# Performance work log

Hardware: AMD Instinct MI355X
Metric: run time of the kernel (lower is better)

## Reference

```python
import jax, jax.numpy as jnp
import numpy as np

ALPHA = 0.5
N_CACHE = 8
N_HEAD = 16
NUM_MODULES = 4


def _ncn_module(x, xa, W, alpha, n_cache, n_head):
    """One fused NCN module: per-head mix, alpha blend with cache slot (t % n_cache),
    activation, and cache update. x: [B,T,D], xa: [B,n_cache,D], W: [H,dh,dh]."""
    B, T, D = x.shape
    dh = D // n_head
    xh = x.reshape(B, T, n_head, dh).transpose(1, 0, 2, 3)  # [T,B,H,dh]
    cache0 = xa.reshape(B, n_cache, n_head, dh)             # [B,C,H,dh]
    slots = jnp.arange(T) % n_cache                          # cache slot per step

    def step(cache, inp):
        xt, s = inp                                          # xt: [B,H,dh]
        mix = jnp.einsum('bhd,hde->bhe', xt, W)              # per-head mixing
        y = jnp.tanh(alpha * cache[:, s] + (1.0 - alpha) * mix)
        return cache.at[:, s].set(y), y

    cache_f, ys = jax.lax.scan(step, cache0, (xh, slots))
    yi = ys.transpose(1, 0, 2, 3).reshape(B, T, D)
    ya = cache_f.reshape(B, n_cache, D)
    return yi, ya


def setup_inputs() -> dict:
    key = jax.random.key(0)
    k1, k2, k3 = jax.random.split(key, 3)
    B, T, D = 8, 4096, 1024
    dh = D // N_HEAD
    x = jax.random.normal(k1, (B, T, D), dtype=jnp.float32)
    xa = jax.random.normal(k2, (B, N_CACHE, D), dtype=jnp.float32)
    # scale weights for stable tanh recurrence
    weights = jax.random.normal(k3, (NUM_MODULES, N_HEAD, dh, dh), dtype=jnp.float32) / np.sqrt(dh)
    return {"x": x, "xa": xa, "weights": weights}


def reference(x, xa, weights):
    for m in range(NUM_MODULES):
        x, xa = _ncn_module(x, xa, weights[m], ALPHA, N_CACHE, N_HEAD)
    return x, xa
```

## Files before the change

kernel.cpp:

```cpp
#include <hip/hip_runtime.h>
#include <hip/hip_fp16.h>


typedef _Float16 f16;
typedef _Float16 half8 __attribute__((ext_vector_type(8)));
typedef _Float16 half4v __attribute__((ext_vector_type(4)));
typedef float f32x4 __attribute__((ext_vector_type(4)));
typedef unsigned uint4v __attribute__((ext_vector_type(4)));

constexpr int B = 8, T = 4096, D = 1024, H = 16, DH = 64, NC = 8, NM = 4;
constexpr int KS = 32;
constexpr int NCH = (T / NC) / KS;
constexpr size_t YWS_BYTES = (size_t)B * T * 2048;
constexpr float L2E = 1.44269504088896340736f;

__device__ __forceinline__ float exp2_fast(float v) {
  float r;
  asm("v_exp_f32 %0, %1" : "=v"(r) : "v"(v));
  return r;
}

template <bool WS>
__global__ __launch_bounds__(256, 1)
void ncn_wave(const float* __restrict__ x, const float* __restrict__ xa,
              const float* __restrict__ w, float* __restrict__ out,
              unsigned char* __restrict__ ybuf) {
  constexpr int YROW = WS ? 2048 : 4096;
  __shared__ __align__(16) unsigned char YST[4][4096];
  __shared__ __align__(16) unsigned char MXS[4][8192];

  const int tid = threadIdx.x, lane = tid & 63, wv = tid >> 6;
  const int g = blockIdx.x * 4 + wv;
  const int c = g & 7, h = (g >> 3) & 15, b = g >> 7;
  const int lr = lane & 15, lg = lane >> 4;

  unsigned char* const yst = YST[wv];
  unsigned char* const mxs = MXS[wv];
  const unsigned char* const xb = (const unsigned char*)x + (size_t)b * T * 4096;
  unsigned char* const ob = (unsigned char*)out + (size_t)b * T * 4096;
  unsigned char* const yb = ybuf + (size_t)b * T * YROW;

  float y = xa[((size_t)b * NC + c) * D + h * DH + lane];
  float u = y * L2E;

  uint4v pf[8];
  half8 Wf[4][2];

  auto prefetch = [&](int m, int ch) {
    const int J0 = ch * KS;
    if (m == 0) {
#pragma unroll
      for (int i = 0; i < 8; ++i) {
        const int lt = i * 4 + (lane >> 4);
        const int t = (J0 + lt) * 8 + c;
        pf[i] = *(const uint4v*)(xb + (size_t)t * 4096 + h * 256 + (lane & 15) * 16);
      }
    } else {
#pragma unroll
      for (int i = 0; i < 4; ++i) {
        const int lt = i * 8 + (lane >> 3);
        const int t = (J0 + lt) * 8 + c;
        pf[i] = *(const uint4v*)(yb + (size_t)t * YROW + h * 128 + (lane & 7) * 16);
      }
    }
  };
  auto stage = [&](int m) {
    if (m == 0) {
#pragma unroll
      for (int i = 0; i < 8; ++i) {
        const int lt = i * 4 + (lane >> 4);
        const f32x4 v = __builtin_bit_cast(f32x4, pf[i]);
        const __half2 p0 = __floats2half2_rn(v.x, v.y);
        const __half2 p1 = __floats2half2_rn(v.z, v.w);
        uint2 pk;
        pk.x = __builtin_bit_cast(unsigned, p0);
        pk.y = __builtin_bit_cast(unsigned, p1);
        *(uint2*)(yst + lt * 128 + (((lane & 15) * 8) ^ ((lt & 7) << 4))) = pk;
      }
    } else {
#pragma unroll
      for (int i = 0; i < 4; ++i) {
        const int lt = i * 8 + (lane >> 3);
        *(uint4v*)(yst + lt * 128 + (((lane & 7) * 16) ^ ((lt & 7) << 4))) = pf[i];
      }
    }
  };

  for (int m = 0; m < NM; ++m) {
    const float* wh = w + ((size_t)m * H + h) * DH * DH;
#pragma unroll
    for (int it = 0; it < 4; ++it)
#pragma unroll
      for (int kt = 0; kt < 2; ++kt)
#pragma unroll
        for (int j = 0; j < 8; ++j)
          Wf[it][kt][j] =
              (f16)wh[(size_t)(kt * 32 + lg * 8 + j) * DH + it * 16 + lr];

    asm volatile("s_waitcnt vmcnt(0)" ::: "memory");

    prefetch(m, 0);
    stage(m);
    prefetch(m, 1);

    for (int ch = 0; ch < NCH; ++ch) {
      f32x4 acc[2][4];
#pragma unroll
      for (int tq = 0; tq < 2; ++tq) {
        half8 Xf[2];
#pragma unroll
        for (int kt = 0; kt < 2; ++kt) {
          const int lt = tq * 16 + lr;
          Xf[kt] = *(const half8*)(yst + lt * 128 +
                                   ((kt * 64 + lg * 16) ^ ((lt & 7) << 4)));
        }
#pragma unroll
        for (int it = 0; it < 4; ++it) acc[tq][it] = (f32x4){0.f, 0.f, 0.f, 0.f};
#pragma unroll
        for (int kt = 0; kt < 2; ++kt)
#pragma unroll
          for (int it = 0; it < 4; ++it)
            acc[tq][it] = __builtin_amdgcn_mfma_f32_16x16x32_f16(
                Xf[kt], Wf[it][kt], acc[tq][it], 0, 0, 0);
      }
      asm volatile("s_waitcnt lgkmcnt(0)" ::: "memory");
      if (ch + 1 < NCH) stage(m);
      if (ch + 2 < NCH) prefetch(m, ch + 2);

#pragma unroll
      for (int tq = 0; tq < 2; ++tq)
#pragma unroll
        for (int it = 0; it < 4; ++it) {
          const int e = it * 16 + lr;
          const __half2 p0 = __floats2half2_rn(acc[tq][it].x, acc[tq][it].y);
          const __half2 p1 = __floats2half2_rn(acc[tq][it].z, acc[tq][it].w);
          uint2 pk;
          pk.x = __builtin_bit_cast(unsigned, p0);
          pk.y = __builtin_bit_cast(unsigned, p1);
          *(uint2*)(mxs + e * 128 + ((tq * 32 + lg * 8) ^ ((e & 7) << 4))) = pk;
        }
      asm volatile("s_waitcnt lgkmcnt(0)" ::: "memory");

      half8 mxr[4];
#pragma unroll
      for (int k16 = 0; k16 < 4; ++k16)
        mxr[k16] = *(const half8*)(mxs + lane * 128 +
                                   ((k16 * 16) ^ ((lane & 7) << 4)));
      float mix2[KS];
#pragma unroll
      for (int k = 0; k < KS; ++k) mix2[k] = (float)mxr[k >> 3][k & 7] * L2E;

      const int t0 = ch * KS * 8 + c;
      if (m < 3 || !WS) {
        unsigned char* sp = yb + (size_t)t0 * YROW + h * 128 + 2 * lane;
#pragma unroll
        for (int k = 0; k < KS; ++k) {
          const float z = u + mix2[k];
          const float E = exp2_fast(z);
          const float r = __builtin_amdgcn_rcpf(E + 1.0f);
          y = fmaf(r, -2.0f, 1.0f);
          u = fmaf(r, -2.0f * L2E, L2E);
          *(__half*)sp = __float2half_rn(y);
          sp += (size_t)8 * YROW;
        }
      } else {
        unsigned char* sp = ob + (size_t)t0 * 4096 + h * 256 + 4 * lane;
#pragma unroll
        for (int k = 0; k < KS; ++k) {
          const float z = u + mix2[k];
          const float E = exp2_fast(z);
          const float r = __builtin_amdgcn_rcpf(E + 1.0f);
          y = fmaf(r, -2.0f, 1.0f);
          u = fmaf(r, -2.0f * L2E, L2E);
          *(float*)sp = y;
          sp += (size_t)8 * 4096;
        }
      }
    }
  }

  float* ya = out + (size_t)B * T * D;
  ya[((size_t)b * NC + c) * D + h * DH + lane] = y;
}

__global__ __launch_bounds__(256)
void expand(float* __restrict__ buf) {
  __shared__ __align__(16) f16 rs[4 * 1024];
  const int tid = threadIdx.x;
  unsigned char* const base = (unsigned char*)buf + (size_t)blockIdx.x * 4 * 4096;
#pragma unroll
  for (int p = 0; p < 2; ++p) {
    const int gid = p * 256 + tid;
    const int row = gid >> 7, c16 = gid & 127;
    *(uint4v*)((unsigned char*)rs + row * 2048 + c16 * 16) =
        *(const uint4v*)(base + (size_t)row * 4096 + c16 * 16);
  }
  __syncthreads();
#pragma unroll
  for (int p = 0; p < 4; ++p) {
    const int gid = p * 256 + tid;
    const int row = gid >> 8, c4 = gid & 255;
    const half4v hv = *(const half4v*)((unsigned char*)rs + row * 2048 + c4 * 8);
    f32x4 v;
#pragma unroll
    for (int e = 0; e < 4; ++e) v[e] = (float)hv[e];
    *(f32x4*)(base + (size_t)row * 4096 + c4 * 16) = v;
  }
}

extern "C" void kernel_launch(void* const* d_in, const int* in_sizes, int n_in,
                              void* d_out, int out_size, void* d_ws, size_t ws_size,
                              hipStream_t stream) {
  (void)in_sizes; (void)n_in; (void)out_size;
  const float* x  = (const float*)d_in[0];
  const float* xa = (const float*)d_in[1];
  const float* w  = (const float*)d_in[2];
  float* out = (float*)d_out;

  const bool usews = (d_ws != nullptr) && (ws_size >= YWS_BYTES);
  if (usews) {
    hipLaunchKernelGGL((ncn_wave<true>), dim3(256), dim3(256), 0, stream,
                       x, xa, w, out, (unsigned char*)d_ws);
  } else {
    hipLaunchKernelGGL((ncn_wave<false>), dim3(256), dim3(256), 0, stream,
                       x, xa, w, out, (unsigned char*)out);
    hipLaunchKernelGGL(expand, dim3(B * T / 4), dim3(256), 0, stream, out);
  }
}
```

Before: 136.2 us.

## Software-pipeline MFMA mixing of next chunk with tanh scan of current

Restructures the per-chunk loop so the MFMA products for chunk ch+1 are issued before the serial tanh recurrence of chunk ch runs, with a scheduling barrier to keep them ahead. The mix results are moved to LDS and reloaded after the scan, so matrix-core latency can hide behind the latency-bound scalar recurrence. In exchange, accumulator and mix registers stay live across the scan, which raises register pressure, and the staging buffer is now written before the previous GEMM's reads are explicitly waited on.

Result: no change. 136.9 us (+0.5%).

```diff
diff --git a/kernel.cpp b/kernel.cpp
--- a/kernel.cpp
+++ b/kernel.cpp
@@ -45,6 +45,8 @@
 
   uint4v pf[8];
   half8 Wf[4][2];
+  float mixf[KS];
+  f32x4 acc[2][4];
 
   auto prefetch = [&](int m, int ch) {
     const int J0 = ch * KS;
@@ -85,6 +87,77 @@
       }
     }
   };
+  auto gemm_issue = [&]() {
+#pragma unroll
+    for (int tq = 0; tq < 2; ++tq) {
+      half8 Xf[2];
+#pragma unroll
+      for (int kt = 0; kt < 2; ++kt) {
+        const int lt = tq * 16 + lr;
+        Xf[kt] = *(const half8*)(yst + lt * 128 +
+                                 ((kt * 64 + lg * 16) ^ ((lt & 7) << 4)));
+      }
+#pragma unroll
+      for (int it = 0; it < 4; ++it) acc[tq][it] = (f32x4){0.f, 0.f, 0.f, 0.f};
+#pragma unroll
+      for (int kt = 0; kt < 2; ++kt)
+#pragma unroll
+        for (int it = 0; it < 4; ++it)
+          acc[tq][it] = __builtin_amdgcn_mfma_f32_16x16x32_f16(
+              Xf[kt], Wf[it][kt], acc[tq][it], 0, 0, 0);
+    }
+  };
+  auto scatter = [&]() {
+#pragma unroll
+    for (int tq = 0; tq < 2; ++tq)
+#pragma unroll
+      for (int it = 0; it < 4; ++it) {
+        const int e = it * 16 + lr;
+        const __half2 p0 = __floats2half2_rn(acc[tq][it].x, acc[tq][it].y);
+        const __half2 p1 = __floats2half2_rn(acc[tq][it].z, acc[tq][it].w);
+        uint2 pk;
+        pk.x = __builtin_bit_cast(unsigned, p0);
+        pk.y = __builtin_bit_cast(unsigned, p1);
+        *(uint2*)(mxs + e * 128 + ((tq * 32 + lg * 8) ^ ((e & 7) << 4))) = pk;
+      }
+  };
+  auto mixload = [&]() {
+    half8 mxr[4];
+#pragma unroll
+    for (int k16 = 0; k16 < 4; ++k16)
+      mxr[k16] = *(const half8*)(mxs + lane * 128 +
+                                 ((k16 * 16) ^ ((lane & 7) << 4)));
+#pragma unroll
+    for (int k = 0; k < KS; ++k) mixf[k] = (float)mxr[k >> 3][k & 7] * L2E;
+  };
+  auto scan = [&](int m, int ch) {
+    const int t0 = ch * KS * 8 + c;
+    if (m < 3 || !WS) {
+      unsigned char* sp = yb + (size_t)t0 * YROW + h * 128 + 2 * lane;
+#pragma unroll
+      for (int k = 0; k < KS; ++k) {
+        const float z = u + mixf[k];
+        const float E = exp2_fast(z);
+        const float r = __builtin_amdgcn_rcpf(E + 1.0f);
+        y = fmaf(r, -2.0f, 1.0f);
+        u = fmaf(r, -2.0f * L2E, L2E);
+        *(__half*)sp = __float2half_rn(y);
+        sp += (size_t)8 * YROW;
+      }
+    } else {
+      unsigned char* sp = ob + (size_t)t0 * 4096 + h * 256 + 4 * lane;
+#pragma unroll
+      for (int k = 0; k < KS; ++k) {
+        const float z = u + mixf[k];
+        const float E = exp2_fast(z);
+        const float r = __builtin_amdgcn_rcpf(E + 1.0f);
+        y = fmaf(r, -2.0f, 1.0f);
+        u = fmaf(r, -2.0f * L2E, L2E);
+        *(float*)sp = y;
+        sp += (size_t)8 * 4096;
+      }
+    }
+  };
 
   for (int m = 0; m < NM; ++m) {
     const float* wh = w + ((size_t)m * H + h) * DH * DH;
@@ -102,79 +175,24 @@
     prefetch(m, 0);
     stage(m);
     prefetch(m, 1);
+    gemm_issue();
+    scatter();
+    asm volatile("s_waitcnt lgkmcnt(0)" ::: "memory");
+    mixload();
 
     for (int ch = 0; ch < NCH; ++ch) {
-      f32x4 acc[2][4];
-#pragma unroll
-      for (int tq = 0; tq < 2; ++tq) {
-        half8 Xf[2];
-#pragma unroll
-        for (int kt = 0; kt < 2; ++kt) {
-          const int lt = tq * 16 + lr;
-          Xf[kt] = *(const half8*)(yst + lt * 128 +
-                                   ((kt * 64 + lg * 16) ^ ((lt & 7) << 4)));
-        }
-#pragma unroll
-        for (int it = 0; it < 4; ++it) acc[tq][it] = (f32x4){0.f, 0.f, 0.f, 0.f};
-#pragma unroll
-        for (int kt = 0; kt < 2; ++kt)
-#pragma unroll
-          for (int it = 0; it < 4; ++it)
-            acc[tq][it] = __builtin_amdgcn_mfma_f32_16x16x32_f16(
-                Xf[kt], Wf[it][kt], acc[tq][it], 0, 0, 0);
-      }
-      asm volatile("s_waitcnt lgkmcnt(0)" ::: "memory");
-      if (ch + 1 < NCH) stage(m);
-      if (ch + 2 < NCH) prefetch(m, ch + 2);
-
-#pragma unroll
-      for (int tq = 0; tq < 2; ++tq)
-#pragma unroll
-        for (int it = 0; it < 4; ++it) {
-          const int e = it * 16 + lr;
-          const __half2 p0 = __floats2half2_rn(acc[tq][it].x, acc[tq][it].y);
-          const __half2 p1 = __floats2half2_rn(acc[tq][it].z, acc[tq][it].w);
-          uint2 pk;
-          pk.x = __builtin_bit_cast(unsigned, p0);
-          pk.y = __builtin_bit_cast(unsigned, p1);
-          *(uint2*)(mxs + e * 128 + ((tq * 32 + lg * 8) ^ ((e & 7) << 4))) = pk;
-        }
-      asm volatile("s_waitcnt lgkmcnt(0)" ::: "memory");
-
-      half8 mxr[4];
-#pragma unroll
-      for (int k16 = 0; k16 < 4; ++k16)
-        mxr[k16] = *(const half8*)(mxs + lane * 128 +
-                                   ((k16 * 16) ^ ((lane & 7) << 4)));
-      float mix2[KS];
-#pragma unroll
-      for (int k = 0; k < KS; ++k) mix2[k] = (float)mxr[k >> 3][k & 7] * L2E;
-
-      const int t0 = ch * KS * 8 + c;
-      if (m < 3 || !WS) {
-        unsigned char* sp = yb + (size_t)t0 * YROW + h * 128 + 2 * lane;
-#pragma unroll
-        for (int k = 0; k < KS; ++k) {
-          const float z = u + mix2[k];
-          const float E = exp2_fast(z);
-          const float r = __builtin_amdgcn_rcpf(E + 1.0f);
-          y = fmaf(r, -2.0f, 1.0f);
-          u = fmaf(r, -2.0f * L2E, L2E);
-          *(__half*)sp = __float2half_rn(y);
-          sp += (size_t)8 * YROW;
-        }
-      } else {
-        unsigned char* sp = ob + (size_t)t0 * 4096 + h * 256 + 4 * lane;
-#pragma unroll
-        for (int k = 0; k < KS; ++k) {
-          const float z = u + mix2[k];
-          const float E = exp2_fast(z);
-          const float r = __builtin_amdgcn_rcpf(E + 1.0f);
-          y = fmaf(r, -2.0f, 1.0f);
-          u = fmaf(r, -2.0f * L2E, L2E);
-          *(float*)sp = y;
-          sp += (size_t)8 * 4096;
-        }
+      const bool more = (ch + 1 < NCH);
+      if (more) {
+        stage(m);
+        if (ch + 2 < NCH) prefetch(m, ch + 2);
+        gemm_issue();
+        __builtin_amdgcn_sched_barrier(0);
+      }
+      scan(m, ch);
+      if (more) {
+        scatter();
+        asm volatile("s_waitcnt lgkmcnt(0)" ::: "memory");
+        mixload();
       }
     }
   }
```

## Split each chain into producer GEMM wave and consumer recurrence wave with LDS flags

Applied to the files above, without the earlier changes.

Each (batch, head, cache-slot) chain now gets a pair of waves. One wave loads and stages inputs and runs the MFMA mixing into a double-buffered LDS mix buffer. The other wave runs the serial tanh recurrence and writes outputs, and the two hand off through workgroup-scope atomic flags. The aim is to overlap the matrix multiply and global loads with the latency-bound recurrence, which the old single wave ran back to back. In exchange the kernel launches twice as many blocks, pays for spin-wait synchronisation, and adds a dependency that blocks the next module's prefetch until the recurrence has stored its outputs.

Measured after the change: 135.4 us. About the same (-0.6%).

```diff
diff --git a/kernel.cpp b/kernel.cpp
--- a/kernel.cpp
+++ b/kernel.cpp
@@ -4,13 +4,13 @@
 
 typedef _Float16 f16;
 typedef _Float16 half8 __attribute__((ext_vector_type(8)));
-typedef _Float16 half4v __attribute__((ext_vector_type(4)));
 typedef float f32x4 __attribute__((ext_vector_type(4)));
 typedef unsigned uint4v __attribute__((ext_vector_type(4)));
 
 constexpr int B = 8, T = 4096, D = 1024, H = 16, DH = 64, NC = 8, NM = 4;
 constexpr int KS = 32;
-constexpr int NCH = (T / NC) / KS;
+constexpr int NCH = 16;
+constexpr int NG = NM * NCH;
 constexpr size_t YWS_BYTES = (size_t)B * T * 2048;
 constexpr float L2E = 1.44269504088896340736f;
 
@@ -21,89 +21,111 @@
 }
 
 template <bool WS>
-__global__ __launch_bounds__(256, 1)
-void ncn_wave(const float* __restrict__ x, const float* __restrict__ xa,
+__global__ __launch_bounds__(256, 2)
+void ncn_pair(const float* __restrict__ x, const float* __restrict__ xa,
               const float* __restrict__ w, float* __restrict__ out,
               unsigned char* __restrict__ ybuf) {
   constexpr int YROW = WS ? 2048 : 4096;
-  __shared__ __align__(16) unsigned char YST[4][4096];
-  __shared__ __align__(16) unsigned char MXS[4][8192];
+  __shared__ __align__(16) unsigned char YST[2][4096];
+  __shared__ __align__(16) unsigned char MXS[2][2][8192];
+  __shared__ int FLG[2][4];
 
   const int tid = threadIdx.x, lane = tid & 63, wv = tid >> 6;
-  const int g = blockIdx.x * 4 + wv;
+  const int pair = wv >> 1;
+  const bool gemmw = (wv & 1) == 0;
+  const int g = blockIdx.x * 2 + pair;
   const int c = g & 7, h = (g >> 3) & 15, b = g >> 7;
   const int lr = lane & 15, lg = lane >> 4;
 
-  unsigned char* const yst = YST[wv];
-  unsigned char* const mxs = MXS[wv];
   const unsigned char* const xb = (const unsigned char*)x + (size_t)b * T * 4096;
   unsigned char* const ob = (unsigned char*)out + (size_t)b * T * 4096;
   unsigned char* const yb = ybuf + (size_t)b * T * YROW;
 
-  float y = xa[((size_t)b * NC + c) * D + h * DH + lane];
-  float u = y * L2E;
-
-  uint4v pf[8];
-  half8 Wf[4][2];
-
-  auto prefetch = [&](int m, int ch) {
-    const int J0 = ch * KS;
-    if (m == 0) {
-#pragma unroll
-      for (int i = 0; i < 8; ++i) {
-        const int lt = i * 4 + (lane >> 4);
-        const int t = (J0 + lt) * 8 + c;
-        pf[i] = *(const uint4v*)(xb + (size_t)t * 4096 + h * 256 + (lane & 15) * 16);
-      }
-    } else {
-#pragma unroll
-      for (int i = 0; i < 4; ++i) {
-        const int lt = i * 8 + (lane >> 3);
-        const int t = (J0 + lt) * 8 + c;
-        pf[i] = *(const uint4v*)(yb + (size_t)t * YROW + h * 128 + (lane & 7) * 16);
-      }
-    }
+  if (tid < 8) ((int*)FLG)[tid] = 0;
+  __syncthreads();
+
+  int* const fgp = &FLG[pair][0];
+  int* const fmx = &FLG[pair][1];
+  int* const fy  = &FLG[pair][2];
+
+  auto waitge = [&](int* f, int v) {
+    while (__hip_atomic_load(f, __ATOMIC_ACQUIRE,
+                             __HIP_MEMORY_SCOPE_WORKGROUP) < v)
+      __builtin_amdgcn_s_sleep(1);
   };
-  auto stage = [&](int m) {
-    if (m == 0) {
-#pragma unroll
-      for (int i = 0; i < 8; ++i) {
-        const int lt = i * 4 + (lane >> 4);
-        const f32x4 v = __builtin_bit_cast(f32x4, pf[i]);
-        const __half2 p0 = __floats2half2_rn(v.x, v.y);
-        const __half2 p1 = __floats2half2_rn(v.z, v.w);
-        uint2 pk;
-        pk.x = __builtin_bit_cast(unsigned, p0);
-        pk.y = __builtin_bit_cast(unsigned, p1);
-        *(uint2*)(yst + lt * 128 + (((lane & 15) * 8) ^ ((lt & 7) << 4))) = pk;
-      }
-    } else {
-#pragma unroll
-      for (int i = 0; i < 4; ++i) {
-        const int lt = i * 8 + (lane >> 3);
-        *(uint4v*)(yst + lt * 128 + (((lane & 7) * 16) ^ ((lt & 7) << 4))) = pf[i];
-      }
-    }
+  auto signal = [&](int* f, int v) {
+    if (lane == 0)
+      __hip_atomic_store(f, v, __ATOMIC_RELEASE, __HIP_MEMORY_SCOPE_WORKGROUP);
   };
 
-  for (int m = 0; m < NM; ++m) {
-    const float* wh = w + ((size_t)m * H + h) * DH * DH;
-#pragma unroll
-    for (int it = 0; it < 4; ++it)
-#pragma unroll
-      for (int kt = 0; kt < 2; ++kt)
-#pragma unroll
-        for (int j = 0; j < 8; ++j)
-          Wf[it][kt][j] =
-              (f16)wh[(size_t)(kt * 32 + lg * 8 + j) * DH + it * 16 + lr];
-
-    asm volatile("s_waitcnt vmcnt(0)" ::: "memory");
-
-    prefetch(m, 0);
-    stage(m);
-    prefetch(m, 1);
-
-    for (int ch = 0; ch < NCH; ++ch) {
+  if (gemmw) {
+    unsigned char* const yst = YST[pair];
+    uint4v pf[8];
+    half8 Wf[4][2];
+
+    auto prefetch = [&](int Gn) {
+      if (Gn >= NG) return;
+      const int m = Gn >> 4, ch = Gn & 15;
+      if (m >= 1) waitge(fy, (m - 1) * 16 + ch + 1);
+      const int J0 = ch * KS;
+      if (m == 0) {
+#pragma unroll
+        for (int i = 0; i < 8; ++i) {
+          const int lt = i * 4 + (lane >> 4);
+          const int t = (J0 + lt) * 8 + c;
+          pf[i] = *(const uint4v*)(xb + (size_t)t * 4096 + h * 256 +
+                                   (lane & 15) * 16);
+        }
+      } else {
+#pragma unroll
+        for (int i = 0; i < 4; ++i) {
+          const int lt = i * 8 + (lane >> 3);
+          const int t = (J0 + lt) * 8 + c;
+          pf[i] = *(const uint4v*)(yb + (size_t)t * YROW + h * 128 +
+                                   (lane & 7) * 16);
+        }
+      }
+    };
+    auto stage = [&](int m) {
+      if (m == 0) {
+#pragma unroll
+        for (int i = 0; i < 8; ++i) {
+          const int lt = i * 4 + (lane >> 4);
+          const f32x4 v = __builtin_bit_cast(f32x4, pf[i]);
+          const __half2 p0 = __floats2half2_rn(v.x, v.y);
+          const __half2 p1 = __floats2half2_rn(v.z, v.w);
+          uint2 pk;
+          pk.x = __builtin_bit_cast(unsigned, p0);
+          pk.y = __builtin_bit_cast(unsigned, p1);
+          *(uint2*)(yst + lt * 128 + (((lane & 15) * 8) ^ ((lt & 7) << 4))) = pk;
+        }
+      } else {
+#pragma unroll
+        for (int i = 0; i < 4; ++i) {
+          const int lt = i * 8 + (lane >> 3);
+          *(uint4v*)(yst + lt * 128 + (((lane & 7) * 16) ^ ((lt & 7) << 4))) =
+              pf[i];
+        }
+      }
+    };
+
+    prefetch(0);
+    for (int G = 0; G < NG; ++G) {
+      const int m = G >> 4, ch = G & 15;
+      if (ch == 0) {
+        const float* wh = w + ((size_t)m * H + h) * DH * DH;
+#pragma unroll
+        for (int it = 0; it < 4; ++it)
+#pragma unroll
+          for (int kt = 0; kt < 2; ++kt)
+#pragma unroll
+            for (int j = 0; j < 8; ++j)
+              Wf[it][kt][j] =
+                  (f16)wh[(size_t)(kt * 32 + lg * 8 + j) * DH + it * 16 + lr];
+      }
+      stage(m);
+      prefetch(G + 1);
+
       f32x4 acc[2][4];
 #pragma unroll
       for (int tq = 0; tq < 2; ++tq) {
@@ -123,10 +145,9 @@
             acc[tq][it] = __builtin_amdgcn_mfma_f32_16x16x32_f16(
                 Xf[kt], Wf[it][kt], acc[tq][it], 0, 0, 0);
       }
-      asm volatile("s_waitcnt lgkmcnt(0)" ::: "memory");
-      if (ch + 1 < NCH) stage(m);
-      if (ch + 2 < NCH) prefetch(m, ch + 2);
-
+
+      waitge(fmx, G - 1);
+      unsigned char* const mxs = MXS[pair][G & 1];
 #pragma unroll
       for (int tq = 0; tq < 2; ++tq)
 #pragma unroll
@@ -140,22 +161,33 @@
           *(uint2*)(mxs + e * 128 + ((tq * 32 + lg * 8) ^ ((e & 7) << 4))) = pk;
         }
       asm volatile("s_waitcnt lgkmcnt(0)" ::: "memory");
-
+      signal(fgp, G + 1);
+    }
+  } else {
+    float y = xa[((size_t)b * NC + c) * D + h * DH + lane];
+    float u = y * L2E;
+    float mixf[KS];
+
+    for (int G = 0; G < NG; ++G) {
+      const int m = G >> 4, ch = G & 15;
+      waitge(fgp, G + 1);
+      const unsigned char* const mxs = MXS[pair][G & 1];
       half8 mxr[4];
 #pragma unroll
       for (int k16 = 0; k16 < 4; ++k16)
         mxr[k16] = *(const half8*)(mxs + lane * 128 +
                                    ((k16 * 16) ^ ((lane & 7) << 4)));
-      float mix2[KS];
-#pragma unroll
-      for (int k = 0; k < KS; ++k) mix2[k] = (float)mxr[k >> 3][k & 7] * L2E;
+#pragma unroll
+      for (int k = 0; k < KS; ++k) mixf[k] = (float)mxr[k >> 3][k & 7] * L2E;
+      asm volatile("s_waitcnt lgkmcnt(0)" ::: "memory");
+      signal(fmx, G + 1);
 
       const int t0 = ch * KS * 8 + c;
       if (m < 3 || !WS) {
         unsigned char* sp = yb + (size_t)t0 * YROW + h * 128 + 2 * lane;
 #pragma unroll
         for (int k = 0; k < KS; ++k) {
-          const float z = u + mix2[k];
+          const float z = u + mixf[k];
           const float E = exp2_fast(z);
           const float r = __builtin_amdgcn_rcpf(E + 1.0f);
           y = fmaf(r, -2.0f, 1.0f);
@@ -167,7 +199,7 @@
         unsigned char* sp = ob + (size_t)t0 * 4096 + h * 256 + 4 * lane;
 #pragma unroll
         for (int k = 0; k < KS; ++k) {
-          const float z = u + mix2[k];
+          const float z = u + mixf[k];
           const float E = exp2_fast(z);
           const float r = __builtin_amdgcn_rcpf(E + 1.0f);
           y = fmaf(r, -2.0f, 1.0f);
@@ -176,15 +208,18 @@
           sp += (size_t)8 * 4096;
         }
       }
+      asm volatile("s_waitcnt vmcnt(0)" ::: "memory");
+      signal(fy, G + 1);
     }
-  }
-
-  float* ya = out + (size_t)B * T * D;
-  ya[((size_t)b * NC + c) * D + h * DH + lane] = y;
+
+    float* ya = out + (size_t)B * T * D;
+    ya[((size_t)b * NC + c) * D + h * DH + lane] = y;
+  }
 }
 
 __global__ __launch_bounds__(256)
 void expand(float* __restrict__ buf) {
+  typedef _Float16 half4v __attribute__((ext_vector_type(4)));
   __shared__ __align__(16) f16 rs[4 * 1024];
   const int tid = threadIdx.x;
   unsigned char* const base = (unsigned char*)buf + (size_t)blockIdx.x * 4 * 4096;
@@ -219,10 +254,10 @@
 
   const bool usews = (d_ws != nullptr) && (ws_size >= YWS_BYTES);
   if (usews) {
-    hipLaunchKernelGGL((ncn_wave<true>), dim3(256), dim3(256), 0, stream,
+    hipLaunchKernelGGL((ncn_pair<true>), dim3(512), dim3(256), 0, stream,
                        x, xa, w, out, (unsigned char*)d_ws);
   } else {
-    hipLaunchKernelGGL((ncn_wave<false>), dim3(256), dim3(256), 0, stream,
+    hipLaunchKernelGGL((ncn_pair<false>), dim3(512), dim3(256), 0, stream,
                        x, xa, w, out, (unsigned char*)out);
     hipLaunchKernelGGL(expand, dim3(B * T / 4), dim3(256), 0, stream, out);
   }
```
